# Performance work log

Hardware: AMD Instinct MI355X
Metric: run time of the kernel (lower is better)

## Reference

```python
import jax, jax.numpy as jnp
import numpy as np

N = 131072        # minibatch nodes
T = 100000        # rows per featured type table
D = 512           # raw feature dim for featured types
E = 256           # embedding size
NUM_NODES = 262144  # total nodes in graph (node embedding table rows)


def setup_inputs() -> dict:
    key = jax.random.key(0)
    ks = jax.random.split(key, 8)
    return {
        "node_ids": jax.random.randint(ks[0], (N,), 0, NUM_NODES),
        "node_tids": jax.random.randint(ks[1], (N,), 0, 4),
        "type_ids": jax.random.randint(ks[2], (N,), 0, T),
        "feats0": jax.random.normal(ks[3], (T, D), dtype=jnp.float32),
        "feats1": jax.random.normal(ks[4], (T, D), dtype=jnp.float32),
        "W0": jax.random.normal(ks[5], (D, E), dtype=jnp.float32) * (6.0 / (D + E)) ** 0.5,
        "W1": jax.random.normal(ks[6], (D, E), dtype=jnp.float32) * (6.0 / (D + E)) ** 0.5,
        "node_emb": jax.random.uniform(ks[7], (NUM_NODES, E), dtype=jnp.float32, minval=-1.0, maxval=1.0),
    }


def reference(node_ids, node_tids, type_ids, feats0, feats1, W0, W1, node_emb):
    # Per-type dispatch: types 0,1 have raw features projected by W_t;
    # types 2,3 read the learnable node-embedding table.
    m0 = (node_tids == 0)
    m1 = (node_tids == 1)
    # safe gather indices (masked-out rows read row 0, then zeroed)
    y0 = (feats0[jnp.where(m0, type_ids, 0)] @ W0) * m0[:, None].astype(W0.dtype)
    y1 = (feats1[jnp.where(m1, type_ids, 0)] @ W1) * m1[:, None].astype(W1.dtype)
    m_emb = jnp.logical_not(m0 | m1)
    ye = node_emb[node_ids] * m_emb[:, None].astype(node_emb.dtype)
    return y0 + y1 + ye  # [N, E]
```

## Files before the change

kernel.cpp:

```cpp
#include <hip/hip_runtime.h>
#include <hip/hip_bf16.h>

typedef __attribute__((ext_vector_type(4))) float f32x4;
typedef __attribute__((ext_vector_type(8))) short bf16x8;

#define NN 131072
#define TT 100000
#define DD 512
#define EE 256

__device__ inline ushort f2bf(float f) {
    union { float f; unsigned u; } x; x.f = f;
    unsigned r = x.u + 0x7fffu + ((x.u >> 16) & 1u);
    return (ushort)(r >> 16);
}

__global__ void compact_kernel(const int* __restrict__ tids, int* __restrict__ cnt,
                               int* __restrict__ l0, int* __restrict__ l1) {
    const int i = blockIdx.x * 256 + threadIdx.x;
    const int t = tids[i];
    const int lane = threadIdx.x & 63, wid = threadIdx.x >> 6;
    unsigned long long b0 = __ballot(t == 0);
    unsigned long long b1 = __ballot(t == 1);
    __shared__ int w0[4], w1[4];
    __shared__ int base0, base1;
    if (lane == 0) { w0[wid] = __popcll(b0); w1[wid] = __popcll(b1); }
    __syncthreads();
    if (threadIdx.x == 0) {
        base0 = atomicAdd(&cnt[0], w0[0] + w0[1] + w0[2] + w0[3]);
        base1 = atomicAdd(&cnt[1], w1[0] + w1[1] + w1[2] + w1[3]);
    }
    __syncthreads();
    int p0 = 0, p1 = 0;
#pragma unroll
    for (int w = 0; w < 4; ++w) if (w < wid) { p0 += w0[w]; p1 += w1[w]; }
    const unsigned long long ltm = (1ull << lane) - 1ull;
    if (t == 0)      l0[base0 + p0 + __popcll(b0 & ltm)] = i;
    else if (t == 1) l1[base1 + p1 + __popcll(b1 & ltm)] = i;
}

__global__ void prep_w_kernel(const float* __restrict__ W0, const float* __restrict__ W1,
                              ushort* __restrict__ Wt0, ushort* __restrict__ Wt1) {
    int gid = blockIdx.x * 256 + threadIdx.x;
    int t = gid >> 15;
    int rem = gid & 32767;
    int d = rem >> 6, eg = rem & 63;
    const float* W = t ? W1 : W0;
    ushort* Wt = t ? Wt1 : Wt0;
    f32x4 v = *(const f32x4*)(W + d * EE + eg * 4);
#pragma unroll
    for (int j = 0; j < 4; ++j)
        Wt[(size_t)(eg * 4 + j) * DD + d] = f2bf(v[j]);
}

__global__ void emb_gather_kernel(const int* __restrict__ ids, const int* __restrict__ tids,
                                  const float* __restrict__ emb, float* __restrict__ out) {
    int gid = blockIdx.x * 256 + threadIdx.x;
    int i = gid >> 6, j = gid & 63;
    if (tids[i] >= 2) {
        ((f32x4*)out)[(size_t)i * 64 + j] = ((const f32x4*)emb)[(size_t)ids[i] * 64 + j];
    }
}

__global__ __launch_bounds__(512) void gemm_gather_kernel(
    const int* __restrict__ list, const int* __restrict__ cntp,
    const int* __restrict__ type_ids, const float* __restrict__ feats,
    const ushort* __restrict__ Wt, float* __restrict__ out) {
    const int cnt = *cntp;
    const int row0 = blockIdx.x * 128;
    if (row0 >= cnt) return;

    __shared__ char Alds[128 * 64 * 2];
    __shared__ char Blds[256 * 64 * 2];

    const int tid = threadIdx.x;
    const int lane = tid & 63, wid = tid >> 6;
    const int wr = wid >> 1, wc = wid & 1;
    const int ln15 = lane & 15, lq = lane >> 4;

    const int ar = tid >> 2, aseg = tid & 3;
    const int rg = row0 + ar;
    int arow = 0;
    if (rg < cnt) arow = type_ids[list[rg]];
    const float* asrc = feats + (size_t)arow * DD + aseg * 16;
    int aw0 = ar * 128 + aseg * 32;
    int aw1 = aw0 + 16;
    aw0 ^= (ar & 7) << 4;
    aw1 ^= (ar & 7) << 4;

    f32x4 acc[2][8] = {};

    for (int k0 = 0; k0 < DD; k0 += 64) {
        const f32x4* ap = (const f32x4*)(asrc + k0);
        f32x4 v0 = ap[0], v1 = ap[1], v2 = ap[2], v3 = ap[3];
        bf16x8 h0, h1;
        h0[0] = (short)f2bf(v0[0]); h0[1] = (short)f2bf(v0[1]);
        h0[2] = (short)f2bf(v0[2]); h0[3] = (short)f2bf(v0[3]);
        h0[4] = (short)f2bf(v1[0]); h0[5] = (short)f2bf(v1[1]);
        h0[6] = (short)f2bf(v1[2]); h0[7] = (short)f2bf(v1[3]);
        h1[0] = (short)f2bf(v2[0]); h1[1] = (short)f2bf(v2[1]);
        h1[2] = (short)f2bf(v2[2]); h1[3] = (short)f2bf(v2[3]);
        h1[4] = (short)f2bf(v3[0]); h1[5] = (short)f2bf(v3[1]);
        h1[6] = (short)f2bf(v3[2]); h1[7] = (short)f2bf(v3[3]);
        *(bf16x8*)(Alds + aw0) = h0;
        *(bf16x8*)(Alds + aw1) = h1;

#pragma unroll
        for (int p = 0; p < 4; ++p) {
            int c = p * 512 + tid;
            int col = c >> 3, seg = c & 7;
            bf16x8 bv = *(const bf16x8*)(Wt + col * DD + k0 + seg * 8);
            int addr = col * 128 + seg * 16;
            addr ^= (col & 7) << 4;
            *(bf16x8*)(Blds + addr) = bv;
        }
        __syncthreads();

#pragma unroll
        for (int kh = 0; kh < 2; ++kh) {
            const int kb = kh * 64 + lq * 16;
            int ra0 = wr * 32 + ln15;
            int a0addr = (ra0 * 128 + kb) ^ ((ra0 & 7) << 4);
            int ra1 = ra0 + 16;
            int a1addr = (ra1 * 128 + kb) ^ ((ra1 & 7) << 4);
            bf16x8 a0 = *(const bf16x8*)(Alds + a0addr);
            bf16x8 a1 = *(const bf16x8*)(Alds + a1addr);
#pragma unroll
            for (int ni = 0; ni < 8; ++ni) {
                int col = wc * 128 + ni * 16 + ln15;
                int baddr = (col * 128 + kb) ^ ((col & 7) << 4);
                bf16x8 b = *(const bf16x8*)(Blds + baddr);
                acc[0][ni] = __builtin_amdgcn_mfma_f32_16x16x32_bf16(a0, b, acc[0][ni], 0, 0, 0);
                acc[1][ni] = __builtin_amdgcn_mfma_f32_16x16x32_bf16(a1, b, acc[1][ni], 0, 0, 0);
            }
        }
        __syncthreads();
    }

#pragma unroll
    for (int mi = 0; mi < 2; ++mi) {
        int mbase = row0 + wr * 32 + mi * 16 + lq * 4;
#pragma unroll
        for (int rr = 0; rr < 4; ++rr) {
            int r = mbase + rr;
            if (r < cnt) {
                int nd = list[r];
                float* orow = out + (size_t)nd * EE + wc * 128 + ln15;
#pragma unroll
                for (int ni = 0; ni < 8; ++ni) orow[ni * 16] = acc[mi][ni][rr];
            }
        }
    }
}

extern "C" void kernel_launch(void* const* d_in, const int* in_sizes, int n_in,
                              void* d_out, int out_size, void* d_ws, size_t ws_size,
                              hipStream_t stream) {
    const int*   node_ids  = (const int*)d_in[0];
    const int*   node_tids = (const int*)d_in[1];
    const int*   type_ids  = (const int*)d_in[2];
    const float* feats0    = (const float*)d_in[3];
    const float* feats1    = (const float*)d_in[4];
    const float* W0        = (const float*)d_in[5];
    const float* W1        = (const float*)d_in[6];
    const float* node_emb  = (const float*)d_in[7];
    float* out = (float*)d_out;

    char* ws = (char*)d_ws;
    int* cnt = (int*)ws;
    int* l0  = (int*)(ws + 16);
    int* l1  = (int*)(ws + 16 + 524288);
    ushort* Wt0 = (ushort*)(ws + 16 + 2 * 524288);
    ushort* Wt1 = Wt0 + DD * EE;

    hipMemsetAsync(cnt, 0, 16, stream);
    prep_w_kernel<<<256, 256, 0, stream>>>(W0, W1, Wt0, Wt1);
    compact_kernel<<<512, 256, 0, stream>>>(node_tids, cnt, l0, l1);
    emb_gather_kernel<<<32768, 256, 0, stream>>>(node_ids, node_tids, node_emb, out);
    gemm_gather_kernel<<<1024, 512, 0, stream>>>(l0, &cnt[0], type_ids, feats0, Wt0, out);
    gemm_gather_kernel<<<1024, 512, 0, stream>>>(l1, &cnt[1], type_ids, feats1, Wt1, out);
}
```

Before: 137.7 us.

## Merge per-type GEMM launches into one grid and fold counter reset into prep

```diff
diff --git a/kernel.cpp b/kernel.cpp
--- a/kernel.cpp
+++ b/kernel.cpp
@@ -40,7 +40,9 @@
 }
 
 __global__ void prep_w_kernel(const float* __restrict__ W0, const float* __restrict__ W1,
-                              ushort* __restrict__ Wt0, ushort* __restrict__ Wt1) {
+                              ushort* __restrict__ Wt0, ushort* __restrict__ Wt1,
+                              int* __restrict__ cnt) {
+    if (blockIdx.x == 0 && threadIdx.x < 4) cnt[threadIdx.x] = 0;
     int gid = blockIdx.x * 256 + threadIdx.x;
     int t = gid >> 15;
     int rem = gid & 32767;
@@ -62,13 +64,21 @@
     }
 }
 
-__global__ __launch_bounds__(512) void gemm_gather_kernel(
-    const int* __restrict__ list, const int* __restrict__ cntp,
-    const int* __restrict__ type_ids, const float* __restrict__ feats,
-    const ushort* __restrict__ Wt, float* __restrict__ out) {
-    const int cnt = *cntp;
-    const int row0 = blockIdx.x * 128;
-    if (row0 >= cnt) return;
+__global__ __launch_bounds__(512, 4) void gemm_gather_kernel(
+    const int* __restrict__ l0, const int* __restrict__ l1,
+    const int* __restrict__ cntp, const int* __restrict__ type_ids,
+    const float* __restrict__ feats0, const float* __restrict__ feats1,
+    const ushort* __restrict__ Wt0, const ushort* __restrict__ Wt1,
+    float* __restrict__ out) {
+    const int cnt0 = cntp[0], cnt1 = cntp[1];
+    const int ntile0 = (cnt0 + 127) >> 7;
+    const int ntile1 = (cnt1 + 127) >> 7;
+    const int b = blockIdx.x;
+    const int* list; const float* feats; const ushort* Wt; int cnt, tile;
+    if (b < ntile0)                { tile = b;          list = l0; feats = feats0; Wt = Wt0; cnt = cnt0; }
+    else if (b < ntile0 + ntile1)  { tile = b - ntile0; list = l1; feats = feats1; Wt = Wt1; cnt = cnt1; }
+    else return;
+    const int row0 = tile * 128;
 
     __shared__ char Alds[128 * 64 * 2];
     __shared__ char Blds[256 * 64 * 2];
@@ -173,10 +183,9 @@
     ushort* Wt0 = (ushort*)(ws + 16 + 2 * 524288);
     ushort* Wt1 = Wt0 + DD * EE;
 
-    hipMemsetAsync(cnt, 0, 16, stream);
-    prep_w_kernel<<<256, 256, 0, stream>>>(W0, W1, Wt0, Wt1);
+    prep_w_kernel<<<256, 256, 0, stream>>>(W0, W1, Wt0, Wt1, cnt);
     compact_kernel<<<512, 256, 0, stream>>>(node_tids, cnt, l0, l1);
     emb_gather_kernel<<<32768, 256, 0, stream>>>(node_ids, node_tids, node_emb, out);
-    gemm_gather_kernel<<<1024, 512, 0, stream>>>(l0, &cnt[0], type_ids, feats0, Wt0, out);
-    gemm_gather_kernel<<<1024, 512, 0, stream>>>(l1, &cnt[1], type_ids, feats1, Wt1, out);
+    gemm_gather_kernel<<<2048, 512, 0, stream>>>(l0, l1, cnt, type_ids,
+                                                 feats0, feats1, Wt0, Wt1, out);
 }
```

Measured after the change: 130.1 us. 5.5% less time.
